# Performance work log

Hardware: AMD Instinct MI355X
Metric: run time of the kernel (lower is better)

## Reference

```python
import jax, jax.numpy as jnp
import numpy as np

B, S, D, H = 2, 2048, 1024, 16
DK = D // H

def setup_inputs() -> dict:
    key = jax.random.key(0)
    k_x, k_q, k_k, k_v, k_o = jax.random.split(key, 5)
    return {
        "x": jax.random.normal(k_x, (B, S, D), dtype=jnp.float32),
        "wq": jax.random.normal(k_q, (D, D), dtype=jnp.float32) * 0.02,
        "wk": jax.random.normal(k_k, (D, D), dtype=jnp.float32) * 0.02,
        "wv": jax.random.normal(k_v, (D, D), dtype=jnp.float32) * 0.02,
        "wo": jax.random.normal(k_o, (D, D), dtype=jnp.float32) * 0.02,
    }

def reference(x, wq, wk, wv, wo):
    b, s, d = x.shape
    # project and split heads: [b, h, s, dk]
    q = (x @ wq).reshape(b, s, H, DK).transpose(0, 2, 1, 3)
    k = (x @ wk).reshape(b, s, H, DK).transpose(0, 2, 1, 3)
    v = (x @ wv).reshape(b, s, H, DK).transpose(0, 2, 1, 3)
    scores = jnp.einsum("bhqd,bhkd->bhqk", q, k) / jnp.sqrt(jnp.float32(DK))
    causal = jnp.tril(jnp.ones((s, s), dtype=bool))  # True = keep
    scores = jnp.where(causal, scores, jnp.finfo(scores.dtype).min)
    probs = jax.nn.softmax(scores, axis=-1)  # dropout pdrop=0.0 -> identity
    out = jnp.einsum("bhqk,bhkd->bhqd", probs, v)
    out = out.transpose(0, 2, 1, 3).reshape(b, s, d)
    return out @ wo
```

## Files before the change

kernel.cpp:

```cpp
#include <hip/hip_runtime.h>
#include <hip/hip_bf16.h>

typedef short s16x8 __attribute__((ext_vector_type(8)));
typedef float f32x4 __attribute__((ext_vector_type(4)));
typedef float f32x16 __attribute__((ext_vector_type(16)));
typedef unsigned short u16x4 __attribute__((ext_vector_type(4)));
typedef unsigned int u32x4 __attribute__((ext_vector_type(4)));

#define D_MODEL 1024
#define N_HEAD  16
#define D_HEAD  64
#define SEQ     2048
#define NBATCH  2

#if __has_builtin(__builtin_amdgcn_exp2f)
#define EXP2(x) __builtin_amdgcn_exp2f(x)
#else
#define EXP2(x) exp2f(x)
#endif

#define GLOAD_LDS16(g, l) \
    __builtin_amdgcn_global_load_lds((const __attribute__((address_space(1))) void*)(g), \
                                     (__attribute__((address_space(3))) void*)(l), 16, 0, 0)

__device__ __forceinline__ unsigned short f2bf(float f) {
    union { float f; unsigned int u; } v; v.f = f;
    unsigned int r = v.u + 0x7FFFu + ((v.u >> 16) & 1u);
    return (unsigned short)(r >> 16);
}

__device__ __forceinline__ float bf2f(unsigned short u) {
    union { unsigned int u; float f; } v; v.u = ((unsigned int)u) << 16;
    return v.f;
}

__device__ __forceinline__ unsigned cvtpk_bf16(float lo, float hi) {
    unsigned r;
    asm("v_cvt_pk_bf16_f32 %0, %1, %2" : "=v"(r) : "v"(lo), "v"(hi));
    return r;
}

__device__ const unsigned char T_S[30] = {5,6,7,8,9,10,11,11,12,12,13,13,14,14,15,15,
                                          4,10, 3,9,15, 2,8,14, 1,7,13, 0,6,12};
__device__ const unsigned char T_C[30] = {0,0,0,0,0,0,0,1,0,1,0,1,0,1,0,1,
                                          0,1, 0,1,2, 0,1,2, 0,1,2, 0,1,2};


__global__ __launch_bounds__(256) void cvt_all_kernel(
    const float* __restrict__ x, unsigned short* __restrict__ xb,
    const float* __restrict__ w0, const float* __restrict__ w1,
    const float* __restrict__ w2, const float* __restrict__ w3,
    unsigned short* __restrict__ o0, unsigned short* __restrict__ o1,
    unsigned short* __restrict__ o2, unsigned short* __restrict__ o3)
{
    __shared__ unsigned short T[64][72];
    const int t = threadIdx.x;
    const int bid = blockIdx.x;
    if (bid < 4096) {
        int i = (bid * 256 + t) * 4;
        float4 v = *reinterpret_cast<const float4*>(x + i);
        u16x4 o;
        o.x = f2bf(v.x); o.y = f2bf(v.y); o.z = f2bf(v.z); o.w = f2bf(v.w);
        *reinterpret_cast<u16x4*>(xb + i) = o;
        return;
    }
    const int u = bid - 4096;
    const int z = u >> 8, tile = u & 255;
    const float* w = (z == 0) ? w0 : (z == 1) ? w1 : (z == 2) ? w2 : w3;
    unsigned short* wt = (z == 0) ? o0 : (z == 1) ? o1 : (z == 2) ? o2 : o3;
    const int k0 = (tile & 15) * 64, n0 = (tile >> 4) * 64;
#pragma unroll
    for (int i = 0; i < 4; ++i) {
        int k = (t >> 4) + i * 16;
        int n = (t & 15) * 4;
        float4 v = *reinterpret_cast<const float4*>(&w[(k0 + k) * 1024 + n0 + n]);
        T[n + 0][k] = f2bf(v.x); T[n + 1][k] = f2bf(v.y);
        T[n + 2][k] = f2bf(v.z); T[n + 3][k] = f2bf(v.w);
    }
    __syncthreads();
#pragma unroll
    for (int i = 0; i < 2; ++i) {
        int n = (t >> 3) + i * 32;
        int kc = (t & 7) * 8;
        *reinterpret_cast<s16x8*>(&wt[(n0 + n) * 1024 + k0 + kc]) =
            *reinterpret_cast<const s16x8*>(&T[n][kc]);
    }
}


__global__ __launch_bounds__(256, 3) void gemm_qkv_kernel(
    const unsigned short* __restrict__ xb,
    const unsigned short* __restrict__ wqt, const unsigned short* __restrict__ wkt,
    const unsigned short* __restrict__ wvt,
    unsigned short* __restrict__ Qb, unsigned short* __restrict__ Kb,
    unsigned short* __restrict__ Vtb)
{
    __shared__ unsigned short As[128 * 64];
    __shared__ unsigned short Bs[128 * 64];
    const int t = threadIdx.x, lane = t & 63, wid = t >> 6;
    const int wr = wid >> 1, wc = wid & 1;
    const int l15 = lane & 15, l4 = lane >> 4;

    const int orig = blockIdx.x;
    const int wg = (orig & 7) * 96 + (orig >> 3);
    const int z = wg >> 8;
    const int rem = wg & 255;
    const int m0 = (rem >> 3) * 128, n0 = (rem & 7) * 128;
    const unsigned short* Bt = (z == 0) ? wqt : (z == 1) ? wkt : wvt;

    const int srow = t >> 3;
    const int srcoff = (((t & 7) ^ (srow & 7)) << 3);
    const unsigned short* Ab = xb + (size_t)(m0 + srow) * D_MODEL + srcoff;
    const unsigned short* Bb = Bt + (size_t)(n0 + srow) * D_MODEL + srcoff;
    const int ldsoff = t * 8;
    const int rsw = l15 & 7;

    f32x4 acc[4][4];
#pragma unroll
    for (int m = 0; m < 4; ++m)
#pragma unroll
        for (int n = 0; n < 4; ++n) acc[m][n] = (f32x4){0.f, 0.f, 0.f, 0.f};

    for (int k0 = 0; k0 < D_MODEL; k0 += 64) {
        __syncthreads();
#pragma unroll
        for (int i = 0; i < 4; ++i) {
            GLOAD_LDS16(Ab + (size_t)(i * 32) * D_MODEL + k0, &As[i * 2048 + ldsoff]);
            GLOAD_LDS16(Bb + (size_t)(i * 32) * D_MODEL + k0, &Bs[i * 2048 + ldsoff]);
        }
        __syncthreads();

#pragma unroll
        for (int ks = 0; ks < 2; ++ks) {
            const int csl = ks * 4 + l4;
            s16x8 af[4], bfr[4];
#pragma unroll
            for (int m = 0; m < 4; ++m)
                af[m] = *reinterpret_cast<const s16x8*>(
                    &As[(wr * 64 + m * 16 + l15) * 64 + ((csl ^ rsw) << 3)]);
#pragma unroll
            for (int n = 0; n < 4; ++n)
                bfr[n] = *reinterpret_cast<const s16x8*>(
                    &Bs[(wc * 64 + n * 16 + l15) * 64 + ((csl ^ rsw) << 3)]);
            __builtin_amdgcn_s_setprio(1);
#pragma unroll
            for (int m = 0; m < 4; ++m)
#pragma unroll
                for (int n = 0; n < 4; ++n)
                    acc[m][n] = __builtin_amdgcn_mfma_f32_16x16x32_bf16(af[m], bfr[n], acc[m][n], 0, 0, 0);
            __builtin_amdgcn_s_setprio(0);
        }
    }

    const int rb = m0 + wr * 64, cb = n0 + wc * 64;
    if (z == 2) {
#pragma unroll
        for (int m = 0; m < 4; ++m) {
            int row = rb + m * 16 + l4 * 4;
            int b = row >> 11, s = row & 2047;
#pragma unroll
            for (int n = 0; n < 4; ++n) {
                int col = cb + n * 16 + l15;
                int h = col >> 6, dk = col & 63;
                u16x4 o;
                o.x = f2bf(acc[m][n][0]); o.y = f2bf(acc[m][n][1]);
                o.z = f2bf(acc[m][n][2]); o.w = f2bf(acc[m][n][3]);
                *reinterpret_cast<u16x4*>(&Vtb[(((b * N_HEAD + h) * D_HEAD + dk) << 11) + s]) = o;
            }
        }
    } else {
        unsigned short* C = (z == 0) ? Qb : Kb;
        const float alpha = (z == 0) ? 0.18033688011112042f : 1.0f;
#pragma unroll
        for (int m = 0; m < 4; ++m)
#pragma unroll
            for (int n = 0; n < 4; ++n)
#pragma unroll
                for (int r = 0; r < 4; ++r)
                    C[(rb + m * 16 + l4 * 4 + r) * D_MODEL + cb + n * 16 + l15] =
                        f2bf(acc[m][n][r] * alpha);
    }
}


__global__ __launch_bounds__(256, 3) void gemm_out_kernel(
    const unsigned short* __restrict__ attnb, const unsigned short* __restrict__ wot,
    float* __restrict__ out)
{
    __shared__ unsigned short As[128 * 64];
    __shared__ unsigned short Bs[64 * 64];
    const int t = threadIdx.x, lane = t & 63, wid = t >> 6;
    const int wr = wid >> 1, wc = wid & 1;
    const int l15 = lane & 15, l4 = lane >> 4;

    const int orig = blockIdx.x;
    const int wg = (orig & 7) * 64 + (orig >> 3);
    const int m0 = (wg >> 4) * 128, n0 = (wg & 15) * 64;

    const int srow = t >> 3;
    const int srcoff = (((t & 7) ^ (srow & 7)) << 3);
    const unsigned short* Ab = attnb + (size_t)(m0 + srow) * D_MODEL + srcoff;
    const unsigned short* Bb = wot + (size_t)(n0 + srow) * D_MODEL + srcoff;
    const int ldsoff = t * 8;
    const int rsw = l15 & 7;

    f32x4 acc[4][2];
#pragma unroll
    for (int m = 0; m < 4; ++m)
#pragma unroll
        for (int n = 0; n < 2; ++n) acc[m][n] = (f32x4){0.f, 0.f, 0.f, 0.f};

    for (int k0 = 0; k0 < D_MODEL; k0 += 64) {
        __syncthreads();
#pragma unroll
        for (int i = 0; i < 4; ++i)
            GLOAD_LDS16(Ab + (size_t)(i * 32) * D_MODEL + k0, &As[i * 2048 + ldsoff]);
#pragma unroll
        for (int i = 0; i < 2; ++i)
            GLOAD_LDS16(Bb + (size_t)(i * 32) * D_MODEL + k0, &Bs[i * 2048 + ldsoff]);
        __syncthreads();

#pragma unroll
        for (int ks = 0; ks < 2; ++ks) {
            const int csl = ks * 4 + l4;
            s16x8 af[4], bfr[2];
#pragma unroll
            for (int m = 0; m < 4; ++m)
                af[m] = *reinterpret_cast<const s16x8*>(
                    &As[(wr * 64 + m * 16 + l15) * 64 + ((csl ^ rsw) << 3)]);
#pragma unroll
            for (int n = 0; n < 2; ++n)
                bfr[n] = *reinterpret_cast<const s16x8*>(
                    &Bs[(wc * 32 + n * 16 + l15) * 64 + ((csl ^ rsw) << 3)]);
            __builtin_amdgcn_s_setprio(1);
#pragma unroll
            for (int m = 0; m < 4; ++m)
#pragma unroll
                for (int n = 0; n < 2; ++n)
                    acc[m][n] = __builtin_amdgcn_mfma_f32_16x16x32_bf16(af[m], bfr[n], acc[m][n], 0, 0, 0);
            __builtin_amdgcn_s_setprio(0);
        }
    }

    const int rb = m0 + wr * 64, cb = n0 + wc * 32;
#pragma unroll
    for (int m = 0; m < 4; ++m)
#pragma unroll
        for (int n = 0; n < 2; ++n)
#pragma unroll
            for (int r = 0; r < 4; ++r)
                out[(rb + m * 16 + l4 * 4 + r) * D_MODEL + cb + n * 16 + l15] = acc[m][n][r];
}


__global__ __launch_bounds__(256, 4) void attn_kernel(
    const unsigned short* __restrict__ Qb, const unsigned short* __restrict__ Kb,
    const unsigned short* __restrict__ Vtb, unsigned short* __restrict__ Ob,
    unsigned short* __restrict__ Opart, float* __restrict__ larr)
{
    __shared__ unsigned short SMEM[8192];
    __shared__ unsigned short SMEMV[8192];

    const int t = threadIdx.x;
    const int lane = t & 63, wid = t >> 6;
    const int l31 = lane & 31, l5 = lane >> 5;

    const int bid = blockIdx.x;
    const int type = bid >> 5, bh = bid & 31;
    const int s = T_S[type], c = T_C[type];
    const int ta = c * 12;
    const int tbf = 2 * (s + 1);
    const int tb = (ta + 12 < tbf) ? ta + 12 : tbf;
    const bool split = (s >= 6);
    const int slot = bh * 24 + ((s < 12) ? (s - 6) * 2 + c : 12 + (s - 12) * 3 + c);

    const int b = bh >> 4, h = bh & 15;
    const int q0 = s << 7;
    const int qw = q0 + wid * 32;
    const int qrow = qw + l31;

    s16x8 qf[4];
#pragma unroll
    for (int ks = 0; ks < 4; ++ks)
        qf[ks] = *reinterpret_cast<const s16x8*>(
            &Qb[(size_t)(b * SEQ + qrow) * D_MODEL + h * D_HEAD + ks * 16 + l5 * 8]);

    f32x16 oacc[2];
#pragma unroll
    for (int d = 0; d < 2; ++d)
#pragma unroll
        for (int r = 0; r < 16; ++r) oacc[d][r] = 0.f;
    float lrun = 0.f;

    const int stK = (wid & 1) * 32;
    const int srow = lane >> 3;
    const int scol = ((lane & 7) ^ srow) * 8;
    const unsigned short* kgb = Kb + (size_t)(b * SEQ + stK + srow) * D_MODEL + h * D_HEAD + scol;
    const unsigned short* vgb = Vtb + ((size_t)(bh * D_HEAD + stK + srow) << 11) + scol;
    const int swz = (l31 & 7);

#define STAGE(bufidx, kvbase) do { \
    if (wid < 2) { \
        const unsigned short* kg = kgb + (size_t)(kvbase) * D_MODEL; \
        _Pragma("unroll") \
        for (int i_ = 0; i_ < 4; ++i_) \
            GLOAD_LDS16(kg + (size_t)(i_ * 8) * D_MODEL, &SMEM[(bufidx) * 4096 + (stK + i_ * 8) * 64]); \
    } else { \
        const unsigned short* vg = vgb + (kvbase); \
        _Pragma("unroll") \
        for (int i_ = 0; i_ < 4; ++i_) \
            GLOAD_LDS16(vg + ((size_t)(i_ * 8) << 11), &SMEMV[(bufidx) * 4096 + (stK + i_ * 8) * 64]); \
    } } while (0)

    STAGE(0, ta * 64);

    for (int ti = ta; ti < tb; ++ti) {
        const int cur = (ti - ta) & 1;
        const int kv0 = ti * 64;
        __builtin_amdgcn_sched_barrier(0);
        asm volatile("s_waitcnt vmcnt(0)" ::: "memory");
        __builtin_amdgcn_s_barrier();
        if (ti + 1 < tb) STAGE(cur ^ 1, (ti + 1) * 64);
        __builtin_amdgcn_sched_barrier(0);

        if (kv0 > qw + 31) continue;

        const unsigned short* KsC = &SMEM[cur * 4096];
        const unsigned short* VsC = &SMEMV[cur * 4096];

        f32x16 sacc[2];
#pragma unroll
        for (int kvsub = 0; kvsub < 2; ++kvsub) {
            const bool active = (kv0 + kvsub * 32 <= qw + 31);
            if (active) {
#pragma unroll
                for (int r = 0; r < 16; ++r) sacc[kvsub][r] = -8.0f;
                __builtin_amdgcn_s_setprio(1);
#pragma unroll
                for (int ks = 0; ks < 4; ++ks) {
                    s16x8 kf = *reinterpret_cast<const s16x8*>(
                        &KsC[(kvsub * 32 + l31) * 64 + (((2 * ks + l5) ^ swz) * 8)]);
                    sacc[kvsub] = __builtin_amdgcn_mfma_f32_32x32x16_bf16(kf, qf[ks], sacc[kvsub], 0, 0, 0);
                }
                __builtin_amdgcn_s_setprio(0);
                if (kv0 + kvsub * 32 + 31 > qw) {
                    int kvbase = kv0 + kvsub * 32 + 4 * l5;
#pragma unroll
                    for (int r = 0; r < 16; ++r) {
                        int kvg = kvbase + (r & 3) + 8 * (r >> 2);
                        sacc[kvsub][r] = (kvg > qrow) ? -1e30f : sacc[kvsub][r];
                    }
                }
#pragma unroll
                for (int r = 0; r < 16; ++r) sacc[kvsub][r] = EXP2(sacc[kvsub][r]);
            } else {
#pragma unroll
                for (int r = 0; r < 16; ++r) sacc[kvsub][r] = 0.f;
            }
        }

        float sred[16];
#pragma unroll
        for (int r = 0; r < 16; ++r) sred[r] = sacc[0][r] + sacc[1][r];
#pragma unroll
        for (int sj = 8; sj >= 1; sj >>= 1)
#pragma unroll
            for (int r = 0; r < 8; ++r)
                if (r < sj) sred[r] += sred[r + sj];
        lrun += sred[0] + __shfl_xor(sred[0], 32);

#pragma unroll
        for (int ks = 0; ks < 4; ++ks) {
            if (kv0 + (ks >> 1) * 32 > qw + 31) continue;
            const int kvsub = ks >> 1, bo = (ks & 1) * 8;
            unsigned a0 = cvtpk_bf16(sacc[kvsub][bo + 0], sacc[kvsub][bo + 1]);
            unsigned a1 = cvtpk_bf16(sacc[kvsub][bo + 2], sacc[kvsub][bo + 3]);
            unsigned a2 = cvtpk_bf16(sacc[kvsub][bo + 4], sacc[kvsub][bo + 5]);
            unsigned a3 = cvtpk_bf16(sacc[kvsub][bo + 6], sacc[kvsub][bo + 7]);
            asm volatile("v_permlane32_swap_b32 %0, %1" : "+v"(a0), "+v"(a2));
            asm volatile("v_permlane32_swap_b32 %0, %1" : "+v"(a1), "+v"(a3));
            u32x4 pw; pw.x = a0; pw.y = a1; pw.z = a2; pw.w = a3;
            s16x8 pf = __builtin_bit_cast(s16x8, pw);
            __builtin_amdgcn_s_setprio(1);
#pragma unroll
            for (int dsub = 0; dsub < 2; ++dsub) {
                s16x8 vf = *reinterpret_cast<const s16x8*>(
                    &VsC[(dsub * 32 + l31) * 64 + (((2 * ks + l5) ^ swz) * 8)]);
                oacc[dsub] = __builtin_amdgcn_mfma_f32_32x32x16_bf16(vf, pf, oacc[dsub], 0, 0, 0);
            }
            __builtin_amdgcn_s_setprio(0);
        }
    }
    __syncthreads();

    float inv = split ? 1.0f : (1.0f / lrun);
    const int orow = wid * 32 + l31;
#pragma unroll
    for (int dsub = 0; dsub < 2; ++dsub)
#pragma unroll
        for (int a = 0; a < 4; ++a) {
            unsigned w0 = cvtpk_bf16(oacc[dsub][4 * a + 0] * inv, oacc[dsub][4 * a + 1] * inv);
            unsigned w1 = cvtpk_bf16(oacc[dsub][4 * a + 2] * inv, oacc[dsub][4 * a + 3] * inv);
            int slt = (4 * dsub + a) ^ (orow & 7);
            uint2 pr; pr.x = w0; pr.y = w1;
            *reinterpret_cast<uint2*>(&SMEM[orow * 64 + slt * 8 + l5 * 4]) = pr;
        }
    __syncthreads();
    if (split) {
        unsigned short* Op = Opart + (size_t)slot * 8192;
#pragma unroll
        for (int i = 0; i < 4; ++i) {
            int g = i * 256 + t;
            int row = g >> 3, c16 = g & 7;
            int cs = (c16 ^ (row & 7)) * 8;
            *reinterpret_cast<s16x8*>(&Op[row * 64 + c16 * 8]) =
                *reinterpret_cast<const s16x8*>(&SMEM[row * 64 + cs]);
        }
        if (l5 == 0) larr[slot * 128 + orow] = lrun;
    } else {
#pragma unroll
        for (int i = 0; i < 4; ++i) {
            int g = i * 256 + t;
            int row = g >> 3, c16 = g & 7;
            int cs = (c16 ^ (row & 7)) * 8;
            s16x8 v = *reinterpret_cast<const s16x8*>(&SMEM[row * 64 + cs]);
            *reinterpret_cast<s16x8*>(
                &Ob[(size_t)(b * SEQ + q0 + row) * D_MODEL + h * D_HEAD + c16 * 8]) = v;
        }
    }
#undef STAGE
}


__global__ __launch_bounds__(256) void combine_kernel(
    const unsigned short* __restrict__ Opart, const float* __restrict__ larr,
    unsigned short* __restrict__ Ob)
{
    const int u = blockIdx.x;
    const int bh = u / 10, s = (u % 10) + 6;
    const int b = bh >> 4, h = bh & 15;
    const int base = bh * 24;
    const int s0 = (s < 12) ? base + (s - 6) * 2 : base + 12 + (s - 12) * 3;
    const int n = (s < 12) ? 2 : 3;
    const int t = threadIdx.x;
#pragma unroll
    for (int i = 0; i < 4; ++i) {
        int g = i * 256 + t;
        int row = g >> 3, c8 = (g & 7) * 8;
        float lsum = larr[s0 * 128 + row] + larr[(s0 + 1) * 128 + row];
        if (n == 3) lsum += larr[(s0 + 2) * 128 + row];
        float inv = 1.0f / lsum;
        float acc[8];
        {
            s16x8 va = *reinterpret_cast<const s16x8*>(&Opart[(size_t)s0 * 8192 + row * 64 + c8]);
            s16x8 vb = *reinterpret_cast<const s16x8*>(&Opart[(size_t)(s0 + 1) * 8192 + row * 64 + c8]);
#pragma unroll
            for (int j = 0; j < 8; ++j)
                acc[j] = bf2f((unsigned short)va[j]) + bf2f((unsigned short)vb[j]);
            if (n == 3) {
                s16x8 vc = *reinterpret_cast<const s16x8*>(&Opart[(size_t)(s0 + 2) * 8192 + row * 64 + c8]);
#pragma unroll
                for (int j = 0; j < 8; ++j) acc[j] += bf2f((unsigned short)vc[j]);
            }
        }
        union { s16x8 v; unsigned short e[8]; } o;
#pragma unroll
        for (int j = 0; j < 8; ++j) o.e[j] = f2bf(acc[j] * inv);
        *reinterpret_cast<s16x8*>(
            &Ob[(size_t)(b * SEQ + s * 128 + row) * D_MODEL + h * D_HEAD + c8]) = o.v;
    }
}


extern "C" void kernel_launch(void* const* d_in, const int* in_sizes, int n_in,
                              void* d_out, int out_size, void* d_ws, size_t ws_size,
                              hipStream_t stream) {
    (void)in_sizes; (void)n_in; (void)out_size; (void)ws_size;
    const float* x  = (const float*)d_in[0];
    const float* wq = (const float*)d_in[1];
    const float* wk = (const float*)d_in[2];
    const float* wv = (const float*)d_in[3];
    const float* wo = (const float*)d_in[4];
    float* out = (float*)d_out;

    char* ws = (char*)d_ws;
    unsigned short* xb  = (unsigned short*)(ws);
    unsigned short* wqt = (unsigned short*)(ws + (8u  << 20));
    unsigned short* wkt = (unsigned short*)(ws + (10u << 20));
    unsigned short* wvt = (unsigned short*)(ws + (12u << 20));
    unsigned short* wot = (unsigned short*)(ws + (14u << 20));
    unsigned short* Qb  = (unsigned short*)(ws + (16u << 20));
    unsigned short* Kb  = (unsigned short*)(ws + (24u << 20));
    unsigned short* Vtb = (unsigned short*)(ws + (32u << 20));
    unsigned short* Ob  = (unsigned short*)(ws + (40u << 20));
    unsigned short* Opart = xb;
    float*          larr  = (float*)wvt;

    hipLaunchKernelGGL(cvt_all_kernel, dim3(5120), dim3(256), 0, stream,
                       x, xb, wq, wk, wv, wo, wqt, wkt, wvt, wot);

    hipLaunchKernelGGL(gemm_qkv_kernel, dim3(768), dim3(256), 0, stream,
                       xb, wqt, wkt, wvt, Qb, Kb, Vtb);
    hipLaunchKernelGGL(attn_kernel, dim3(960), dim3(256), 0, stream,
                       Qb, Kb, Vtb, Ob, Opart, larr);
    hipLaunchKernelGGL(combine_kernel, dim3(320), dim3(256), 0, stream, Opart, larr, Ob);
    hipLaunchKernelGGL(gemm_out_kernel, dim3(512), dim3(256), 0, stream, Ob, wot, out);
}
```

Measured before the change: 97.29 us.

## Fuse split-KV combine into output GEMM and compute row sums via MFMA

Removes the separate combine kernel: the output projection GEMM now, for split query tiles, reads the partial attention outputs and row sums, normalizes and sums them, and writes the bf16 A tile into shared memory itself instead of using async global-to-LDS loads. In the attention kernel, the per-row softmax denominator is accumulated with an extra MFMA against a ones matrix instead of a shuffle and add reduction. This saves one kernel launch and an extra round trip of the combined output through global memory. In exchange, split tiles do synchronous loads and conversion work inside the GEMM main loop, and the attention inner loop issues one extra MFMA per step.

```diff
diff --git a/kernel.cpp b/kernel.cpp
--- a/kernel.cpp
+++ b/kernel.cpp
@@ -184,8 +184,9 @@
 
 
 __global__ __launch_bounds__(256, 3) void gemm_out_kernel(
-    const unsigned short* __restrict__ attnb, const unsigned short* __restrict__ wot,
-    float* __restrict__ out)
+    const unsigned short* __restrict__ attnb,
+    const unsigned short* __restrict__ Opart, const float* __restrict__ larr,
+    const unsigned short* __restrict__ wot, float* __restrict__ out)
 {
     __shared__ unsigned short As[128 * 64];
     __shared__ unsigned short Bs[64 * 64];
@@ -197,8 +198,14 @@
     const int wg = (orig & 7) * 64 + (orig >> 3);
     const int m0 = (wg >> 4) * 128, n0 = (wg & 15) * 64;
 
+    const int bq = m0 >> 11, sst = (m0 & 2047) >> 7;
+    const bool split = (sst >= 6);
+    const int soff = (sst < 12) ? (sst - 6) * 2 : 12 + (sst - 12) * 3;
+    const int nsl = (sst < 12) ? 2 : 3;
+
     const int srow = t >> 3;
-    const int srcoff = (((t & 7) ^ (srow & 7)) << 3);
+    const int cg = t & 7;
+    const int srcoff = ((cg ^ (srow & 7)) << 3);
     const unsigned short* Ab = attnb + (size_t)(m0 + srow) * D_MODEL + srcoff;
     const unsigned short* Bb = wot + (size_t)(n0 + srow) * D_MODEL + srcoff;
     const int ldsoff = t * 8;
@@ -212,9 +219,39 @@
 
     for (int k0 = 0; k0 < D_MODEL; k0 += 64) {
         __syncthreads();
-#pragma unroll
-        for (int i = 0; i < 4; ++i)
-            GLOAD_LDS16(Ab + (size_t)(i * 32) * D_MODEL + k0, &As[i * 2048 + ldsoff]);
+        if (!split) {
+#pragma unroll
+            for (int i = 0; i < 4; ++i)
+                GLOAD_LDS16(Ab + (size_t)(i * 32) * D_MODEL + k0, &As[i * 2048 + ldsoff]);
+        } else {
+            const int h = k0 >> 6;
+            const int slot0 = (bq * 16 + h) * 24 + soff;
+#pragma unroll
+            for (int i = 0; i < 4; ++i) {
+                const int row = i * 32 + srow;
+                float lsum = larr[slot0 * 128 + row] + larr[(slot0 + 1) * 128 + row];
+                if (nsl == 3) lsum += larr[(slot0 + 2) * 128 + row];
+                const float inv = 1.0f / lsum;
+                const unsigned short* pa = Opart + (size_t)slot0 * 8192 + row * 64 + cg * 8;
+                s16x8 va = *reinterpret_cast<const s16x8*>(pa);
+                s16x8 vb = *reinterpret_cast<const s16x8*>(pa + 8192);
+                float sm[8];
+#pragma unroll
+                for (int j = 0; j < 8; ++j)
+                    sm[j] = bf2f((unsigned short)va[j]) + bf2f((unsigned short)vb[j]);
+                if (nsl == 3) {
+                    s16x8 vc = *reinterpret_cast<const s16x8*>(pa + 16384);
+#pragma unroll
+                    for (int j = 0; j < 8; ++j) sm[j] += bf2f((unsigned short)vc[j]);
+                }
+                u32x4 pw;
+                pw.x = cvtpk_bf16(sm[0] * inv, sm[1] * inv);
+                pw.y = cvtpk_bf16(sm[2] * inv, sm[3] * inv);
+                pw.z = cvtpk_bf16(sm[4] * inv, sm[5] * inv);
+                pw.w = cvtpk_bf16(sm[6] * inv, sm[7] * inv);
+                *reinterpret_cast<u32x4*>(&As[row * 64 + srcoff]) = pw;
+            }
+        }
 #pragma unroll
         for (int i = 0; i < 2; ++i)
             GLOAD_LDS16(Bb + (size_t)(i * 32) * D_MODEL + k0, &Bs[i * 2048 + ldsoff]);
@@ -285,12 +322,16 @@
         qf[ks] = *reinterpret_cast<const s16x8*>(
             &Qb[(size_t)(b * SEQ + qrow) * D_MODEL + h * D_HEAD + ks * 16 + l5 * 8]);
 
-    f32x16 oacc[2];
+    const short oneb = (short)0x3F80;
+    const s16x8 onesf = {oneb, oneb, oneb, oneb, oneb, oneb, oneb, oneb};
+
+    f32x16 oacc[2], lacc;
 #pragma unroll
     for (int d = 0; d < 2; ++d)
 #pragma unroll
         for (int r = 0; r < 16; ++r) oacc[d][r] = 0.f;
-    float lrun = 0.f;
+#pragma unroll
+    for (int r = 0; r < 16; ++r) lacc[r] = 0.f;
 
     const int stK = (wid & 1) * 32;
     const int srow = lane >> 3;
@@ -359,16 +400,6 @@
             }
         }
 
-        float sred[16];
-#pragma unroll
-        for (int r = 0; r < 16; ++r) sred[r] = sacc[0][r] + sacc[1][r];
-#pragma unroll
-        for (int sj = 8; sj >= 1; sj >>= 1)
-#pragma unroll
-            for (int r = 0; r < 8; ++r)
-                if (r < sj) sred[r] += sred[r + sj];
-        lrun += sred[0] + __shfl_xor(sred[0], 32);
-
 #pragma unroll
         for (int ks = 0; ks < 4; ++ks) {
             if (kv0 + (ks >> 1) * 32 > qw + 31) continue;
@@ -382,6 +413,7 @@
             u32x4 pw; pw.x = a0; pw.y = a1; pw.z = a2; pw.w = a3;
             s16x8 pf = __builtin_bit_cast(s16x8, pw);
             __builtin_amdgcn_s_setprio(1);
+            lacc = __builtin_amdgcn_mfma_f32_32x32x16_bf16(onesf, pf, lacc, 0, 0, 0);
 #pragma unroll
             for (int dsub = 0; dsub < 2; ++dsub) {
                 s16x8 vf = *reinterpret_cast<const s16x8*>(
@@ -393,6 +425,7 @@
     }
     __syncthreads();
 
+    const float lrun = lacc[0];
     float inv = split ? 1.0f : (1.0f / lrun);
     const int orow = wid * 32 + l31;
 #pragma unroll
@@ -429,46 +462,6 @@
         }
     }
 #undef STAGE
-}
-
-
-__global__ __launch_bounds__(256) void combine_kernel(
-    const unsigned short* __restrict__ Opart, const float* __restrict__ larr,
-    unsigned short* __restrict__ Ob)
-{
-    const int u = blockIdx.x;
-    const int bh = u / 10, s = (u % 10) + 6;
-    const int b = bh >> 4, h = bh & 15;
-    const int base = bh * 24;
-    const int s0 = (s < 12) ? base + (s - 6) * 2 : base + 12 + (s - 12) * 3;
-    const int n = (s < 12) ? 2 : 3;
-    const int t = threadIdx.x;
-#pragma unroll
-    for (int i = 0; i < 4; ++i) {
-        int g = i * 256 + t;
-        int row = g >> 3, c8 = (g & 7) * 8;
-        float lsum = larr[s0 * 128 + row] + larr[(s0 + 1) * 128 + row];
-        if (n == 3) lsum += larr[(s0 + 2) * 128 + row];
-        float inv = 1.0f / lsum;
-        float acc[8];
-        {
-            s16x8 va = *reinterpret_cast<const s16x8*>(&Opart[(size_t)s0 * 8192 + row * 64 + c8]);
-            s16x8 vb = *reinterpret_cast<const s16x8*>(&Opart[(size_t)(s0 + 1) * 8192 + row * 64 + c8]);
-#pragma unroll
-            for (int j = 0; j < 8; ++j)
-                acc[j] = bf2f((unsigned short)va[j]) + bf2f((unsigned short)vb[j]);
-            if (n == 3) {
-                s16x8 vc = *reinterpret_cast<const s16x8*>(&Opart[(size_t)(s0 + 2) * 8192 + row * 64 + c8]);
-#pragma unroll
-                for (int j = 0; j < 8; ++j) acc[j] += bf2f((unsigned short)vc[j]);
-            }
-        }
-        union { s16x8 v; unsigned short e[8]; } o;
-#pragma unroll
-        for (int j = 0; j < 8; ++j) o.e[j] = f2bf(acc[j] * inv);
-        *reinterpret_cast<s16x8*>(
-            &Ob[(size_t)(b * SEQ + s * 128 + row) * D_MODEL + h * D_HEAD + c8]) = o.v;
-    }
 }
 
 
@@ -503,6 +496,6 @@
                        xb, wqt, wkt, wvt, Qb, Kb, Vtb);
     hipLaunchKernelGGL(attn_kernel, dim3(960), dim3(256), 0, stream,
                        Qb, Kb, Vtb, Ob, Opart, larr);
-    hipLaunchKernelGGL(combine_kernel, dim3(320), dim3(256), 0, stream, Opart, larr, Ob);
-    hipLaunchKernelGGL(gemm_out_kernel, dim3(512), dim3(256), 0, stream, Ob, wot, out);
-}
+    hipLaunchKernelGGL(gemm_out_kernel, dim3(512), dim3(256), 0, stream,
+                       Ob, Opart, larr, wot, out);
+}
```

New measurement: 160.8 us. +65.2%, slower.
